# Optimization experiments

Hardware: AMD Instinct MI355X
Metric: run time of the kernel (lower is better)

The kernel has to match this reference:

```python
import jax, jax.numpy as jnp
import numpy as np

# ---- static configuration (mirrors init_kwargs) ----
B, NCAM = 1, 6
FC, FH, FW = 128, 16, 44              # featureShape
ORFH, ORFW = 128, 352                 # transformedImgShape H, W
D_ST, D_END, D_STEP = 1.0, 49.0, 1.0
D = int(np.arange(D_ST, D_END, D_STEP).shape[0])   # 48 depth bins
OUTC = 128
XB = (-50.0, 50.0, 1.0)
YB = (-50.0, 50.0, 1.0)
BEV_H = int((YB[1] - YB[0]) / YB[2])  # 100
BEV_W = int((XB[1] - XB[0]) / XB[2])  # 100
THRESH = 0.05                         # opacity_filter
ERR_TOL = 1.0                         # error_tolerance
COV_DILATE = 0.3                      # 3DGS low-pass on 2D cov diagonal
ALPHA_MAX = 0.99
ALPHA_MIN = 1.0 / 255.0
BN_EPS = 1e-3


def _frustum():
    ds = jnp.arange(D_ST, D_END, D_STEP, dtype=jnp.float32)[:, None, None]
    xs = jnp.linspace(0.0, ORFW - 1.0, FW, dtype=jnp.float32)[None, None, :]
    ys = jnp.linspace(0.0, ORFH - 1.0, FH, dtype=jnp.float32)[None, :, None]
    shp = (D, FH, FW)
    return jnp.stack([jnp.broadcast_to(xs, shp), jnp.broadcast_to(ys, shp),
                      jnp.broadcast_to(ds, shp)], axis=-1)  # [D,FH,FW,3]


def _conv(x, w, b, pad):
    y = jax.lax.conv_general_dilated(x, w, (1, 1), [(pad, pad), (pad, pad)],
                                     dimension_numbers=('NCHW', 'OIHW', 'NCHW'))
    return y + b[None, :, None, None]


def _bn(x, g, beta, m, v):
    # eval-mode BatchNorm2d with running stats
    inv = g / jnp.sqrt(v + BN_EPS)
    return (x - m[None, :, None, None]) * inv[None, :, None, None] + beta[None, :, None, None]


def _rasterize(features, means, cov6, opac):
    """Differentiable BEV Gaussian splatting (alpha compositing in index order).
    features [G,C], means [G,3] (normalized to [-1,1]), cov6 [G,6]=(xx,xy,xz,yy,yz,zz), opac [G].
    """
    h, w = BEV_H, BEV_W
    sh, sw = h / 2.0, w / 2.0                 # h/FoVy, w/FoVx with FoV=2
    op = jnp.where(opac > THRESH, opac, 0.0)  # opacity cull (variable-length mask in torch)
    # full_proj_transform: row0 -> row index (y), row1 -> col index (x)
    py = h / 2.0 - sh * means[:, 1]
    px = w / 2.0 - sw * means[:, 0]
    # 2D covariance in (py,px) basis: J Sigma3 J^T with J = [[0,-sh,0],[-sw,0,0]]
    a = sh * sh * cov6[:, 3] + COV_DILATE     # var along py (from Sigma_yy)
    b = sh * sw * cov6[:, 1]                  # cov(py,px) (from Sigma_xy)
    c = sw * sw * cov6[:, 0] + COV_DILATE     # var along px (from Sigma_xx)
    det = a * c - b * b
    op = jnp.where(det > 0.0, op, 0.0)
    inv_det = 1.0 / jnp.where(det > 0.0, det, 1.0)
    ys = jnp.arange(h, dtype=jnp.float32)
    xs = jnp.arange(w, dtype=jnp.float32)
    dy = py[None, :] - ys[:, None]            # [h,G]
    dx = px[None, :] - xs[:, None]            # [w,G]
    # power = -0.5 d^T Sigma2^{-1} d, Sigma2^{-1} = [[c,-b],[-b,a]]/det
    power = (-0.5 * (c * inv_det) * dy * dy)[:, None, :] \
            + (-0.5 * (a * inv_det) * dx * dx)[None, :, :] \
            + (b * inv_det) * dy[:, None, :] * dx[None, :, :]   # [h,w,G]
    alpha = jnp.minimum(ALPHA_MAX, op * jnp.exp(jnp.minimum(power, 0.0)))
    alpha = jnp.where(alpha < ALPHA_MIN, 0.0, alpha)
    T = jnp.cumprod(1.0 - alpha, axis=-1)
    T_excl = jnp.concatenate([jnp.ones_like(T[..., :1]), T[..., :-1]], axis=-1)
    wgt = alpha * T_excl                      # [h,w,G]
    bev = jnp.einsum('hwg,gc->chw', wgt, features)   # bg color = 0
    return bev


def reference(cam2ego_rot, cam2ego_trans, cam_intrins, post_cam2ego_rot, post_cam2ego_trans,
              img_feats, conv1_w, conv1_b, bn1_g, bn1_b, bn1_m, bn1_v,
              conv2_w, conv2_b, bn2_g, bn2_b, bn2_m, bn2_v, conv3_w, conv3_b):
    # --- geometry lifting ---
    frustum = _frustum()                                             # [D,FH,FW,3]
    pts = frustum[None, None] - post_cam2ego_trans[:, :, None, None, None, :]
    pts = jnp.einsum('bnij,bndhwj->bndhwi', jnp.linalg.inv(post_cam2ego_rot), pts)
    pts = jnp.concatenate([pts[..., :2] * pts[..., 2:3], pts[..., 2:3]], axis=-1)
    combine = cam2ego_rot @ jnp.linalg.inv(cam_intrins)
    geometry = jnp.einsum('bnij,bndhwj->bndhwi', combine, pts) \
               + cam2ego_trans[:, :, None, None, None, :]            # [B,N,D,FH,FW,3]
    # --- depth net ---
    x = img_feats.reshape(B * NCAM, FC, FH, FW)
    x = jax.nn.relu(_bn(_conv(x, conv1_w, conv1_b, 1), bn1_g, bn1_b, bn1_m, bn1_v))
    x = jax.nn.relu(_bn(_conv(x, conv2_w, conv2_b, 1), bn2_g, bn2_b, bn2_m, bn2_v))
    x = _conv(x, conv3_w, conv3_b, 0)                                # [B*N, OUTC+D+1, H, W]
    depth_prob = jax.nn.softmax(x[:, :D], axis=1).reshape(B, NCAM, D, FH, FW)
    opac = jax.nn.sigmoid(x[:, D:D + 1]).reshape(B, NCAM, FH, FW)
    feats = x[:, D + 1:].reshape(B, NCAM, OUTC, FH, FW)
    # --- per-pixel Gaussian moments over the depth distribution ---
    means3d = jnp.einsum('bndhw,bndhwi->bnhwi', depth_prob, geometry)
    delta = means3d[:, :, None] - geometry                           # [B,N,D,FH,FW,3]
    cov = jnp.einsum('bndhw,bndhwi,bndhwj->bnhwij', depth_prob, delta, delta)
    cov = cov * (ERR_TOL ** 2 / 9.0)
    # --- normalize to BEV frame ---
    center = jnp.array([(XB[0] + XB[1]) / 2.0, (YB[0] + YB[1]) / 2.0, 0.0], jnp.float32)
    scale = jnp.array([2.0 / (XB[1] - XB[0]), 2.0 / (YB[1] - YB[0]), 1.0], jnp.float32)
    means_n = (means3d - center) * scale
    cov_n = cov * (scale[:, None] * scale[None, :])
    cov6 = jnp.stack([cov_n[..., 0, 0], cov_n[..., 0, 1], cov_n[..., 0, 2],
                      cov_n[..., 1, 1], cov_n[..., 1, 2], cov_n[..., 2, 2]], axis=-1)
    G = NCAM * FH * FW
    f = jnp.transpose(feats, (0, 1, 3, 4, 2)).reshape(B, G, OUTC)
    m = means_n.reshape(B, G, 3)
    c6 = cov6.reshape(B, G, 6)
    o = opac.reshape(B, G)
    bev = jax.vmap(_rasterize)(f, m, c6, o)                          # [B,OUTC,BEV_H,BEV_W]
    return bev


def setup_inputs() -> dict:
    key = jax.random.key(0)
    ks = jax.random.split(key, 16)
    eye = jnp.eye(3, dtype=jnp.float32)
    cam2ego_rot = eye + 0.05 * jax.random.normal(ks[0], (B, NCAM, 3, 3), jnp.float32)
    cam2ego_trans = 0.5 * jax.random.normal(ks[1], (B, NCAM, 3), jnp.float32)
    intr = jnp.array([[260.0, 0.0, ORFW / 2.0], [0.0, 260.0, ORFH / 2.0], [0.0, 0.0, 1.0]], jnp.float32)
    cam_intrins = jnp.broadcast_to(intr, (B, NCAM, 3, 3)) * (1.0 + 0.01 * jax.random.normal(ks[2], (B, NCAM, 1, 1), jnp.float32))
    post_cam2ego_rot = eye + 0.01 * jax.random.normal(ks[3], (B, NCAM, 3, 3), jnp.float32)
    post_cam2ego_trans = 2.0 * jax.random.normal(ks[4], (B, NCAM, 3), jnp.float32)
    img_feats = jax.random.normal(ks[5], (B, NCAM, FC, FH, FW), jnp.float32)
    def cw(k, o, i, kh, kw):
        return jax.random.normal(k, (o, i, kh, kw), jnp.float32) / np.sqrt(i * kh * kw)
    inp = dict(cam2ego_rot=cam2ego_rot, cam2ego_trans=cam2ego_trans, cam_intrins=cam_intrins,
               post_cam2ego_rot=post_cam2ego_rot, post_cam2ego_trans=post_cam2ego_trans,
               img_feats=img_feats,
               conv1_w=cw(ks[6], FC, FC, 3, 3), conv1_b=jnp.zeros((FC,), jnp.float32),
               bn1_g=jnp.ones((FC,), jnp.float32), bn1_b=0.1 * jax.random.normal(ks[7], (FC,), jnp.float32),
               bn1_m=jnp.zeros((FC,), jnp.float32), bn1_v=jnp.ones((FC,), jnp.float32),
               conv2_w=cw(ks[8], FC, FC, 3, 3), conv2_b=jnp.zeros((FC,), jnp.float32),
               bn2_g=jnp.ones((FC,), jnp.float32), bn2_b=0.1 * jax.random.normal(ks[9], (FC,), jnp.float32),
               bn2_m=jnp.zeros((FC,), jnp.float32), bn2_v=jnp.ones((FC,), jnp.float32),
               conv3_w=cw(ks[10], OUTC + D + 1, FC, 1, 1),
               conv3_b=jnp.zeros((OUTC + D + 1,), jnp.float32))
    return inp
```

## Files before the change

kernel.cpp:

```cpp
#include <hip/hip_runtime.h>
#include <math.h>

#define NCAM 6
#define FHh 16
#define FWw 44
#define PIX 704
#define FCc 128
#define DB 48
#define C3 177
#define KCONV 1152
#define NG 4224
#define BEVN 10000
#define NSPLIT 3
#define SG 1408
#define TH_LOG (-5.5412635f)

#define OFF_WT1    0
#define OFF_WT2    147456
#define OFF_WT3    294912
#define OFF_GEO    319488
#define OFF_X1     724992
#define OFF_X2     1265664
#define OFF_X3     1806336
#define OFF_PART   2553984
#define OFF_PRM    4716672
#define OFF_PRM2   4733568
#define OFF_FEATT  4742016
#define OFF_SF     0
#define OFF_SP     3840000

typedef __attribute__((ext_vector_type(8))) short bf16x8;
typedef __attribute__((ext_vector_type(4))) float f32x4;
typedef __attribute__((ext_vector_type(4))) int i32x4;

__device__ __forceinline__ unsigned short f2bf(float x) {
  unsigned u = __float_as_uint(x);
  return (unsigned short)((u + 0x7FFF + ((u >> 16) & 1)) >> 16);
}
__device__ __forceinline__ float bf2f(unsigned short h) {
  return __uint_as_float(((unsigned)h) << 16);
}

__device__ __forceinline__ void inv3(const float* A, float* I) {
  float a=A[0],b=A[1],c=A[2],d=A[3],e=A[4],f=A[5],g=A[6],h=A[7],i=A[8];
  float c0 = e*i - f*h, c1 = f*g - d*i, c2 = d*h - e*g;
  float det = a*c0 + b*c1 + c*c2;
  float id = 1.f/det;
  I[0]=c0*id; I[1]=(c*h-b*i)*id; I[2]=(b*f-c*e)*id;
  I[3]=c1*id; I[4]=(a*i-c*g)*id; I[5]=(c*d-a*f)*id;
  I[6]=c2*id; I[7]=(b*g-a*h)*id; I[8]=(a*e-b*d)*id;
}

__global__ void k_prep(const float* __restrict__ rot, const float* __restrict__ intr,
                       const float* __restrict__ post_rot,
                       const float* __restrict__ trans, const float* __restrict__ post_trans,
                       const float* __restrict__ w1, const float* __restrict__ w2,
                       const float* __restrict__ w3, float* __restrict__ ws) {
  if (blockIdx.x < 792) {
    __shared__ float sm[NCAM][24];
    if (threadIdx.x < NCAM) {
      int n = threadIdx.x;
      float ip[9], ii[9];
      inv3(post_rot + n*9, ip);
      inv3(intr + n*9, ii);
      const float* R = rot + n*9;
      for (int j = 0; j < 9; ++j) sm[n][j] = ip[j];
      for (int r = 0; r < 3; ++r)
        for (int c = 0; c < 3; ++c) {
          float s = 0.f;
          for (int k = 0; k < 3; ++k) s += R[r*3+k]*ii[k*3+c];
          sm[n][9 + r*3 + c] = s;
        }
    }
    __syncthreads();
    int idx = blockIdx.x*256 + threadIdx.x;
    if (idx >= NCAM*DB*PIX) return;
    int n = idx / (DB*PIX);
    int rem = idx % (DB*PIX);
    int d = rem / PIX;
    int hw = rem % PIX;
    int h = hw / FWw, w = hw % FWw;
    float fx = w * (351.0f/43.0f);
    float fy = h * (127.0f/15.0f);
    float fz = 1.0f + (float)d;
    const float* pt = post_trans + n*3;
    float v0 = fx - pt[0], v1 = fy - pt[1], v2 = fz - pt[2];
    const float* m = sm[n];
    float x = m[0]*v0 + m[1]*v1 + m[2]*v2;
    float y = m[3]*v0 + m[4]*v1 + m[5]*v2;
    float z = m[6]*v0 + m[7]*v1 + m[8]*v2;
    float q0 = x*z, q1 = y*z, q2 = z;
    const float* c = m + 9;
    const float* t = trans + n*3;
    float gx = c[0]*q0 + c[1]*q1 + c[2]*q2 + t[0];
    float gy = c[3]*q0 + c[4]*q1 + c[5]*q2 + t[1];
    ((float2*)(ws + OFF_GEO))[idx] = make_float2(gx, gy);
  } else {
    int e = (blockIdx.x - 792)*256 + threadIdx.x;
    if (e < 147456) {
      float v1 = w1[e], v2 = w2[e];
      unsigned short h1 = f2bf(v1), h2 = f2bf(v2);
      unsigned short l1 = f2bf(v1 - bf2f(h1)), l2 = f2bf(v2 - bf2f(h2));
      unsigned short* wt1 = (unsigned short*)(ws + OFF_WT1);
      unsigned short* wt2 = (unsigned short*)(ws + OFF_WT2);
      wt1[e] = h1; wt1[147456 + e] = l1;
      wt2[e] = h2; wt2[147456 + e] = l2;
    }
    if (e < 192*128) {
      int oc = e >> 7, k = e & 127;
      float v = (oc < C3) ? w3[oc*FCc + k] : 0.f;
      unsigned short h = f2bf(v);
      unsigned short* wt3 = (unsigned short*)(ws + OFF_WT3);
      wt3[e] = h; wt3[24576 + e] = f2bf(v - bf2f(h));
    }
  }
}

#define LROW 20

__global__ __launch_bounds__(256) void k_gemm_mfma(
    const float* __restrict__ in, const float* ws, float* __restrict__ part, int woff)
{
  __shared__ int alds[2][64*LROW];
  __shared__ int blds[2][64*LROW];
  int tid = threadIdx.x;
  int px0 = blockIdx.x * 64;
  int oc0 = blockIdx.y * 64;
  int z = blockIdx.z; int n = z >> 2, ks = z & 3;
  const unsigned short* whi = (const unsigned short*)(ws + woff);
  const unsigned short* wlo = whi + 147456;
  const float* inn = in + (size_t)n*FCc*PIX;
  int wv = tid >> 6, lane = tid & 63;
  int a_oc = tid >> 2, a_kq = tid & 3;
  int b_px = tid & 63, b_kq = tid >> 6;
  int p = px0 + b_px; int b_y = p / FWw, b_x = p - b_y*FWw;
  int k00 = ks * 288;

  i32x4 pa_h, pa_l; float bv[8];
  auto issueA = [&](int s) {
    size_t gi = (size_t)(oc0 + a_oc)*KCONV + (k00 + s*32 + a_kq*8);
    pa_h = *(const i32x4*)(whi + gi);
    pa_l = *(const i32x4*)(wlo + gi);
  };
  auto issueB = [&](int s) {
    #pragma unroll
    for (int j = 0; j < 8; ++j) {
      int k = k00 + s*32 + b_kq*8 + j;
      int ic = k / 9, tap = k - ic*9;
      int ky = tap / 3, kx = tap - ky*3;
      int yy = b_y + ky - 1, xx = b_x + kx - 1;
      float v = 0.f;
      if ((unsigned)yy < FHh && (unsigned)xx < FWw) v = inn[(size_t)ic*PIX + yy*FWw + xx];
      bv[j] = v;
    }
  };

  f32x4 a00 = {0.f,0.f,0.f,0.f}, a01 = a00, a10 = a00, a11 = a00;
  int ocr = (wv >> 1) * 32, pxr = (wv & 1) * 32;
  int dq = (lane >> 4) * 4;
  int rA0 = (ocr + (lane & 15)) * LROW + dq;
  int rA1 = rA0 + 16*LROW;
  int rB0 = (pxr + (lane & 15)) * LROW + dq;
  int rB1 = rB0 + 16*LROW;
  int aw = a_oc*LROW + a_kq*4;
  int bw = b_px*LROW + b_kq*4;

  issueA(0); issueB(0);
  for (int s = 0; s < 9; ++s) {
    __syncthreads();
    *(i32x4*)&alds[0][aw] = pa_h;
    *(i32x4*)&alds[1][aw] = pa_l;
    {
      i32x4 vh, vl;
      int th[8], tl[8];
      #pragma unroll
      for (int j = 0; j < 8; ++j) {
        unsigned short h = f2bf(bv[j]);
        th[j] = h; tl[j] = f2bf(bv[j] - bf2f(h));
      }
      vh.x = th[0]|(th[1]<<16); vh.y = th[2]|(th[3]<<16);
      vh.z = th[4]|(th[5]<<16); vh.w = th[6]|(th[7]<<16);
      vl.x = tl[0]|(tl[1]<<16); vl.y = tl[2]|(tl[3]<<16);
      vl.z = tl[4]|(tl[5]<<16); vl.w = tl[6]|(tl[7]<<16);
      *(i32x4*)&blds[0][bw] = vh;
      *(i32x4*)&blds[1][bw] = vl;
    }
    __syncthreads();
    if (s < 8) { issueA(s+1); issueB(s+1); }
    bf16x8 ah0 = *(bf16x8*)&alds[0][rA0], ah1 = *(bf16x8*)&alds[0][rA1];
    bf16x8 al0 = *(bf16x8*)&alds[1][rA0], al1 = *(bf16x8*)&alds[1][rA1];
    bf16x8 bh0 = *(bf16x8*)&blds[0][rB0], bh1 = *(bf16x8*)&blds[0][rB1];
    bf16x8 bl0 = *(bf16x8*)&blds[1][rB0], bl1 = *(bf16x8*)&blds[1][rB1];
    a00 = __builtin_amdgcn_mfma_f32_16x16x32_bf16(ah0, bh0, a00, 0, 0, 0);
    a01 = __builtin_amdgcn_mfma_f32_16x16x32_bf16(ah0, bh1, a01, 0, 0, 0);
    a10 = __builtin_amdgcn_mfma_f32_16x16x32_bf16(ah1, bh0, a10, 0, 0, 0);
    a11 = __builtin_amdgcn_mfma_f32_16x16x32_bf16(ah1, bh1, a11, 0, 0, 0);
    a00 = __builtin_amdgcn_mfma_f32_16x16x32_bf16(ah0, bl0, a00, 0, 0, 0);
    a01 = __builtin_amdgcn_mfma_f32_16x16x32_bf16(ah0, bl1, a01, 0, 0, 0);
    a10 = __builtin_amdgcn_mfma_f32_16x16x32_bf16(ah1, bl0, a10, 0, 0, 0);
    a11 = __builtin_amdgcn_mfma_f32_16x16x32_bf16(ah1, bl1, a11, 0, 0, 0);
    a00 = __builtin_amdgcn_mfma_f32_16x16x32_bf16(al0, bh0, a00, 0, 0, 0);
    a01 = __builtin_amdgcn_mfma_f32_16x16x32_bf16(al0, bh1, a01, 0, 0, 0);
    a10 = __builtin_amdgcn_mfma_f32_16x16x32_bf16(al1, bh0, a10, 0, 0, 0);
    a11 = __builtin_amdgcn_mfma_f32_16x16x32_bf16(al1, bh1, a11, 0, 0, 0);
  }
  float* pp = part + (size_t)(ks*NCAM + n)*FCc*PIX;
  int ocb = oc0 + ocr + ((lane >> 4) << 2);
  int pxb = px0 + pxr + (lane & 15);
  #pragma unroll
  for (int i = 0; i < 4; ++i) {
    pp[(size_t)(ocb + i)*PIX + pxb]           = a00[i];
    pp[(size_t)(ocb + i)*PIX + pxb + 16]      = a01[i];
    pp[(size_t)(ocb + 16 + i)*PIX + pxb]      = a10[i];
    pp[(size_t)(ocb + 16 + i)*PIX + pxb + 16] = a11[i];
  }
}

__global__ __launch_bounds__(256) void k_gemm_mfma3(
    const float* __restrict__ in, const float* ws,
    const float* __restrict__ bias, float* __restrict__ outbuf)
{
  __shared__ int alds[2][64*LROW];
  __shared__ int blds[2][64*LROW];
  int tid = threadIdx.x;
  int px0 = blockIdx.x * 64;
  int oc0 = blockIdx.y * 64;
  int n = blockIdx.z;
  const unsigned short* whi = (const unsigned short*)(ws + OFF_WT3);
  const unsigned short* wlo = whi + 24576;
  const float* inn = in + (size_t)n*FCc*PIX;
  int wv = tid >> 6, lane = tid & 63;
  int a_oc = tid >> 2, a_kq = tid & 3;
  int b_px = tid & 63, b_kq = tid >> 6;
  int p = px0 + b_px;

  i32x4 pa_h, pa_l; float bvv[8];
  auto issueA = [&](int s) {
    size_t gi = (size_t)(oc0 + a_oc)*128 + (s*32 + a_kq*8);
    pa_h = *(const i32x4*)(whi + gi);
    pa_l = *(const i32x4*)(wlo + gi);
  };
  auto issueB = [&](int s) {
    #pragma unroll
    for (int j = 0; j < 8; ++j) {
      int ic = s*32 + b_kq*8 + j;
      bvv[j] = inn[(size_t)ic*PIX + p];
    }
  };

  f32x4 a00 = {0.f,0.f,0.f,0.f}, a01 = a00, a10 = a00, a11 = a00;
  int ocr = (wv >> 1) * 32, pxr = (wv & 1) * 32;
  int dq = (lane >> 4) * 4;
  int rA0 = (ocr + (lane & 15)) * LROW + dq;
  int rA1 = rA0 + 16*LROW;
  int rB0 = (pxr + (lane & 15)) * LROW + dq;
  int rB1 = rB0 + 16*LROW;
  int aw = a_oc*LROW + a_kq*4;
  int bw = b_px*LROW + b_kq*4;

  issueA(0); issueB(0);
  for (int s = 0; s < 4; ++s) {
    __syncthreads();
    *(i32x4*)&alds[0][aw] = pa_h;
    *(i32x4*)&alds[1][aw] = pa_l;
    {
      i32x4 vh, vl;
      int th[8], tl[8];
      #pragma unroll
      for (int j = 0; j < 8; ++j) {
        unsigned short h = f2bf(bvv[j]);
        th[j] = h; tl[j] = f2bf(bvv[j] - bf2f(h));
      }
      vh.x = th[0]|(th[1]<<16); vh.y = th[2]|(th[3]<<16);
      vh.z = th[4]|(th[5]<<16); vh.w = th[6]|(th[7]<<16);
      vl.x = tl[0]|(tl[1]<<16); vl.y = tl[2]|(tl[3]<<16);
      vl.z = tl[4]|(tl[5]<<16); vl.w = tl[6]|(tl[7]<<16);
      *(i32x4*)&blds[0][bw] = vh;
      *(i32x4*)&blds[1][bw] = vl;
    }
    __syncthreads();
    if (s < 3) { issueA(s+1); issueB(s+1); }
    bf16x8 ah0 = *(bf16x8*)&alds[0][rA0], ah1 = *(bf16x8*)&alds[0][rA1];
    bf16x8 al0 = *(bf16x8*)&alds[1][rA0], al1 = *(bf16x8*)&alds[1][rA1];
    bf16x8 bh0 = *(bf16x8*)&blds[0][rB0], bh1 = *(bf16x8*)&blds[0][rB1];
    bf16x8 bl0 = *(bf16x8*)&blds[1][rB0], bl1 = *(bf16x8*)&blds[1][rB1];
    a00 = __builtin_amdgcn_mfma_f32_16x16x32_bf16(ah0, bh0, a00, 0, 0, 0);
    a01 = __builtin_amdgcn_mfma_f32_16x16x32_bf16(ah0, bh1, a01, 0, 0, 0);
    a10 = __builtin_amdgcn_mfma_f32_16x16x32_bf16(ah1, bh0, a10, 0, 0, 0);
    a11 = __builtin_amdgcn_mfma_f32_16x16x32_bf16(ah1, bh1, a11, 0, 0, 0);
    a00 = __builtin_amdgcn_mfma_f32_16x16x32_bf16(ah0, bl0, a00, 0, 0, 0);
    a01 = __builtin_amdgcn_mfma_f32_16x16x32_bf16(ah0, bl1, a01, 0, 0, 0);
    a10 = __builtin_amdgcn_mfma_f32_16x16x32_bf16(ah1, bl0, a10, 0, 0, 0);
    a11 = __builtin_amdgcn_mfma_f32_16x16x32_bf16(ah1, bl1, a11, 0, 0, 0);
    a00 = __builtin_amdgcn_mfma_f32_16x16x32_bf16(al0, bh0, a00, 0, 0, 0);
    a01 = __builtin_amdgcn_mfma_f32_16x16x32_bf16(al0, bh1, a01, 0, 0, 0);
    a10 = __builtin_amdgcn_mfma_f32_16x16x32_bf16(al1, bh0, a10, 0, 0, 0);
    a11 = __builtin_amdgcn_mfma_f32_16x16x32_bf16(al1, bh1, a11, 0, 0, 0);
  }
  int ocb = oc0 + ocr + ((lane >> 4) << 2);
  int pxb = px0 + pxr + (lane & 15);
  #pragma unroll
  for (int i = 0; i < 4; ++i) {
    int o0 = ocb + i, o1 = ocb + 16 + i;
    if (o0 < C3) {
      float b = bias[o0];
      outbuf[(size_t)(n*C3 + o0)*PIX + pxb]      = a00[i] + b;
      outbuf[(size_t)(n*C3 + o0)*PIX + pxb + 16] = a01[i] + b;
    }
    if (o1 < C3) {
      float b = bias[o1];
      outbuf[(size_t)(n*C3 + o1)*PIX + pxb]      = a10[i] + b;
      outbuf[(size_t)(n*C3 + o1)*PIX + pxb + 16] = a11[i] + b;
    }
  }
}

__global__ void k_epi_bn(const float* __restrict__ part, const float* __restrict__ cb,
                         const float* __restrict__ g, const float* __restrict__ be,
                         const float* __restrict__ mn, const float* __restrict__ vr,
                         float* __restrict__ out, int KSPLIT)
{
  int idx = blockIdx.x*256 + threadIdx.x;
  if (idx >= NCAM*FCc*176) return;
  int px4 = idx % 176;
  int t = idx / 176;
  int oc = t % FCc;
  int n = t / FCc;
  float4 s = {0.f,0.f,0.f,0.f};
  for (int ks = 0; ks < KSPLIT; ++ks) {
    const float4* p = (const float4*)(part + (size_t)((ks*NCAM+n)*FCc + oc)*PIX);
    float4 v = p[px4];
    s.x += v.x; s.y += v.y; s.z += v.z; s.w += v.w;
  }
  float inv = g[oc] * rsqrtf(vr[oc] + 1e-3f);
  float sh = (cb[oc] - mn[oc]) * inv + be[oc];
  float4 o;
  o.x = fmaxf(s.x*inv + sh, 0.f);
  o.y = fmaxf(s.y*inv + sh, 0.f);
  o.z = fmaxf(s.z*inv + sh, 0.f);
  o.w = fmaxf(s.w*inv + sh, 0.f);
  ((float4*)(out + (size_t)(n*FCc + oc)*PIX))[px4] = o;
}

__global__ void k_moments(float* __restrict__ ws) {
  int wid  = (blockIdx.x * 256 + threadIdx.x) >> 6;
  int lane = threadIdx.x & 63;
  int n = wid / PIX, hw = wid % PIX;
  const float* x3 = ws + OFF_X3 + (size_t)n*C3*PIX + hw;
  float logit = (lane < DB) ? x3[(size_t)lane*PIX] : -1e30f;
  float mx = logit;
  for (int off = 1; off < 64; off <<= 1) mx = fmaxf(mx, __shfl_xor(mx, off));
  float e = (lane < DB) ? expf(logit - mx) : 0.f;
  float s = e;
  for (int off = 1; off < 64; off <<= 1) s += __shfl_xor(s, off);
  float p = e / s;
  float gx = 0.f, gy = 0.f;
  if (lane < DB) {
    float2 g2 = ((const float2*)(ws + OFF_GEO))[(size_t)(n*DB + lane)*PIX + hw];
    gx = g2.x; gy = g2.y;
  }
  float sx = p*gx;
  for (int off = 1; off < 64; off <<= 1) sx += __shfl_xor(sx, off);
  float sy = p*gy;
  for (int off = 1; off < 64; off <<= 1) sy += __shfl_xor(sy, off);
  float dx = gx - sx, dy = gy - sy;
  float c00 = p*dx*dx, c01 = p*dx*dy, c11 = p*dy*dy;
  for (int off = 1; off < 64; off <<= 1) c00 += __shfl_xor(c00, off);
  for (int off = 1; off < 64; off <<= 1) c01 += __shfl_xor(c01, off);
  for (int off = 1; off < 64; off <<= 1) c11 += __shfl_xor(c11, off);
  float opl = x3[(size_t)DB*PIX];
  float opac = 1.f / (1.f + expf(-opl));
  float a = c11*(1.f/9.f) + 0.3f;
  float b = c01*(1.f/9.f);
  float c = c00*(1.f/9.f) + 0.3f;
  float py = 50.f - sy;
  float px = 50.f - sx;
  float det = a*c - b*b;
  float op = (opac > 0.05f) ? opac : 0.f;
  float invd = 1.f;
  if (det > 0.f) invd = 1.f/det; else op = 0.f;
  if (lane == 0) {
    float lop = (op > 0.f) ? logf(op) : -1e30f;
    ((float4*)(ws + OFF_PRM))[wid]  = make_float4(py, px, -0.5f*c*invd, -0.5f*a*invd);
    ((float2*)(ws + OFF_PRM2))[wid] = make_float2(b*invd, lop);
  }
  float* ft = ws + OFF_FEATT + (size_t)wid*128;
  ft[lane]      = x3[(size_t)(DB + 1 + lane)*PIX];
  ft[lane + 64] = x3[(size_t)(DB + 1 + lane + 64)*PIX];
}

template<int CTRL, int RMASK>
__device__ __forceinline__ float dpp_mul(float v) {
  int t = __builtin_amdgcn_update_dpp(0x3f800000, __float_as_int(v), CTRL, RMASK, 0xF, false);
  return v * __int_as_float(t);
}

__global__ __launch_bounds__(512) void k_raster(const float* __restrict__ ws,
                                                float* __restrict__ wsout) {
  __shared__ float4 s4[SG];
  __shared__ float2 s2[SG];
  int lane = threadIdx.x & 63, wv = threadIdx.x >> 6;
  int split = blockIdx.x / 1250;
  int pxb   = blockIdx.x % 1250;
  int pix = pxb * 8 + wv;
  float yi = (float)(pix / 100), xi = (float)(pix % 100);
  int gbase = split * SG;
  const float4* prm4 = (const float4*)(ws + OFF_PRM) + gbase;
  const float2* prm2 = (const float2*)(ws + OFF_PRM2) + gbase;
  const float2* ft = (const float2*)(ws + OFF_FEATT);
  for (int i = threadIdx.x; i < SG; i += 512) {
    s4[i] = prm4[i];
    s2[i] = prm2[i];
  }
  __syncthreads();
  float T = 1.f, ax = 0.f, ay = 0.f;
  for (int gl = 0; gl < SG; gl += 64) {
    float4 c4 = s4[gl + lane];
    float2 c2 = s2[gl + lane];
    float dyv = c4.x - yi, dxv = c4.y - xi;
    float pw = c4.z*dyv*dyv + c4.w*dxv*dxv + c2.x*dyv*dxv;
    float t  = pw + c2.y;
    bool hit = (t >= TH_LOG);
    unsigned long long m0 = __ballot(hit);
    if (m0) {
      float alpha = __expf(fminf(t, c2.y));
      alpha = fminf(alpha, 0.99f);
      alpha = hit ? alpha : 0.f;
      float P = 1.f - alpha;
      P = dpp_mul<0x111, 0xF>(P);
      P = dpp_mul<0x112, 0xF>(P);
      P = dpp_mul<0x114, 0xF>(P);
      P = dpp_mul<0x118, 0xF>(P);
      P = dpp_mul<0x142, 0xA>(P);
      P = dpp_mul<0x143, 0xC>(P);
      float E = __int_as_float(__builtin_amdgcn_update_dpp(
                  0x3f800000, __float_as_int(P), 0x138, 0xF, 0xF, false));
      float w = alpha * T * E;
      T *= __int_as_float(__builtin_amdgcn_readlane(__float_as_int(P), 63));
      unsigned long long mask = __ballot(w > 1e-9f);
      int g0 = gbase + gl;
      while (mask) {
        int jj[8];
        #pragma unroll
        for (int b = 0; b < 8; ++b) {
          if (mask) { jj[b] = __builtin_ctzll(mask); mask &= mask - 1ull; }
          else jj[b] = -1;
        }
        float2 fb[8]; float wb[8];
        #pragma unroll
        for (int b = 0; b < 8; ++b) {
          int j = (jj[b] >= 0) ? jj[b] : jj[0];
          fb[b] = ft[(size_t)(g0 + j)*64 + lane];
          wb[b] = (jj[b] >= 0)
            ? __int_as_float(__builtin_amdgcn_readlane(__float_as_int(w), jj[b]))
            : 0.f;
        }
        #pragma unroll
        for (int b = 0; b < 8; ++b) { ax += wb[b]*fb[b].x; ay += wb[b]*fb[b].y; }
      }
      if (T < 1e-7f) break;
    }
  }
  unsigned* sfu = (unsigned*)(wsout + OFF_SF);
  sfu[((size_t)split*BEVN + pix)*64 + lane] =
      (unsigned)f2bf(ax) | ((unsigned)f2bf(ay) << 16);
  if (lane == 0) (wsout + OFF_SP)[split*BEVN + pix] = T;
}

__global__ __launch_bounds__(512) void k_combine(const float* __restrict__ ws,
                                                 float* __restrict__ out) {
  int lane = threadIdx.x & 63, wv = threadIdx.x >> 6;
  int pix = blockIdx.x * 8 + wv;
  const float* sp = ws + OFF_SP;
  float P0 = sp[pix], P1 = sp[BEVN + pix];
  const unsigned* sfu = (const unsigned*)(ws + OFF_SF);
  unsigned u0 = sfu[(size_t)pix*64 + lane];
  unsigned u1 = sfu[((size_t)BEVN + pix)*64 + lane];
  unsigned u2 = sfu[((size_t)2*BEVN + pix)*64 + lane];
  float w1 = P0, w2 = P0*P1;
  float ox = bf2f((unsigned short)(u0 & 0xffff))
           + w1*bf2f((unsigned short)(u1 & 0xffff))
           + w2*bf2f((unsigned short)(u2 & 0xffff));
  float oy = bf2f((unsigned short)(u0 >> 16))
           + w1*bf2f((unsigned short)(u1 >> 16))
           + w2*bf2f((unsigned short)(u2 >> 16));
  out[(size_t)(2*lane)*BEVN + pix]   = ox;
  out[(size_t)(2*lane+1)*BEVN + pix] = oy;
}

extern "C" void kernel_launch(void* const* d_in, const int* in_sizes, int n_in,
                              void* d_out, int out_size, void* d_ws, size_t ws_size,
                              hipStream_t stream) {
  const float* rot        = (const float*)d_in[0];
  const float* trans      = (const float*)d_in[1];
  const float* intr       = (const float*)d_in[2];
  const float* post_rot   = (const float*)d_in[3];
  const float* post_trans = (const float*)d_in[4];
  const float* img        = (const float*)d_in[5];
  const float* w1  = (const float*)d_in[6];
  const float* b1  = (const float*)d_in[7];
  const float* g1  = (const float*)d_in[8];
  const float* be1 = (const float*)d_in[9];
  const float* m1  = (const float*)d_in[10];
  const float* v1  = (const float*)d_in[11];
  const float* w2  = (const float*)d_in[12];
  const float* b2  = (const float*)d_in[13];
  const float* g2  = (const float*)d_in[14];
  const float* be2 = (const float*)d_in[15];
  const float* m2  = (const float*)d_in[16];
  const float* v2  = (const float*)d_in[17];
  const float* w3  = (const float*)d_in[18];
  const float* b3  = (const float*)d_in[19];
  float* ws  = (float*)d_ws;
  float* out = (float*)d_out;

  k_prep<<<1368, 256, 0, stream>>>(rot, intr, post_rot, trans, post_trans,
                                   w1, w2, w3, ws);

  k_gemm_mfma<<<dim3(11,2,24), 256, 0, stream>>>(img, ws, ws+OFF_PART, OFF_WT1);
  k_epi_bn<<<528, 256, 0, stream>>>(ws+OFF_PART, b1, g1, be1, m1, v1, ws+OFF_X1, 4);
  k_gemm_mfma<<<dim3(11,2,24), 256, 0, stream>>>(ws+OFF_X1, ws, ws+OFF_PART, OFF_WT2);
  k_epi_bn<<<528, 256, 0, stream>>>(ws+OFF_PART, b2, g2, be2, m2, v2, ws+OFF_X2, 4);
  k_gemm_mfma3<<<dim3(11,3,6), 256, 0, stream>>>(ws+OFF_X2, ws, b3, ws+OFF_X3);

  k_moments<<<1056, 256, 0, stream>>>(ws);
  k_raster<<<3750, 512, 0, stream>>>(ws, ws);
  k_combine<<<1250, 512, 0, stream>>>(ws, out);
}
```

Measured before the change: 119.8 us.

## Restructure moments kernel to pixel-per-lane with coalesced loads and LDS transpose

The moments kernel now maps 64 consecutive pixels to lanes and splits the 48 depth bins across 4 waves. Softmax and moment reductions go through shared memory instead of 64-lane shuffle trees, and the feature transpose is staged through an LDS tile so both the reads and the writes are coalesced. This removes the strided per-wave gathers and the many shuffle reductions. The trade-off is that the grid drops from 1056 blocks to 66, so fewer CUs are occupied.

```diff
diff --git a/kernel.cpp b/kernel.cpp
--- a/kernel.cpp
+++ b/kernel.cpp
@@ -342,51 +342,85 @@
   ((float4*)(out + (size_t)(n*FCc + oc)*PIX))[px4] = o;
 }
 
-__global__ void k_moments(float* __restrict__ ws) {
-  int wid  = (blockIdx.x * 256 + threadIdx.x) >> 6;
-  int lane = threadIdx.x & 63;
-  int n = wid / PIX, hw = wid % PIX;
-  const float* x3 = ws + OFF_X3 + (size_t)n*C3*PIX + hw;
-  float logit = (lane < DB) ? x3[(size_t)lane*PIX] : -1e30f;
-  float mx = logit;
-  for (int off = 1; off < 64; off <<= 1) mx = fmaxf(mx, __shfl_xor(mx, off));
-  float e = (lane < DB) ? expf(logit - mx) : 0.f;
-  float s = e;
-  for (int off = 1; off < 64; off <<= 1) s += __shfl_xor(s, off);
-  float p = e / s;
-  float gx = 0.f, gy = 0.f;
-  if (lane < DB) {
-    float2 g2 = ((const float2*)(ws + OFF_GEO))[(size_t)(n*DB + lane)*PIX + hw];
-    gx = g2.x; gy = g2.y;
-  }
-  float sx = p*gx;
-  for (int off = 1; off < 64; off <<= 1) sx += __shfl_xor(sx, off);
-  float sy = p*gy;
-  for (int off = 1; off < 64; off <<= 1) sy += __shfl_xor(sy, off);
-  float dx = gx - sx, dy = gy - sy;
-  float c00 = p*dx*dx, c01 = p*dx*dy, c11 = p*dy*dy;
-  for (int off = 1; off < 64; off <<= 1) c00 += __shfl_xor(c00, off);
-  for (int off = 1; off < 64; off <<= 1) c01 += __shfl_xor(c01, off);
-  for (int off = 1; off < 64; off <<= 1) c11 += __shfl_xor(c11, off);
-  float opl = x3[(size_t)DB*PIX];
-  float opac = 1.f / (1.f + expf(-opl));
-  float a = c11*(1.f/9.f) + 0.3f;
-  float b = c01*(1.f/9.f);
-  float c = c00*(1.f/9.f) + 0.3f;
-  float py = 50.f - sy;
-  float px = 50.f - sx;
-  float det = a*c - b*b;
-  float op = (opac > 0.05f) ? opac : 0.f;
-  float invd = 1.f;
-  if (det > 0.f) invd = 1.f/det; else op = 0.f;
-  if (lane == 0) {
+__global__ __launch_bounds__(256) void k_moments(float* __restrict__ ws) {
+  __shared__ float r0[4][64], r1[4][64], r2[4][64];
+  __shared__ float tile[64][65];
+  int tid = threadIdx.x;
+  int w = tid >> 6, l = tid & 63;
+  int n = blockIdx.x / 11, hw0 = (blockIdx.x % 11) * 64;
+  int hw = hw0 + l;
+  const float* x3 = ws + OFF_X3 + (size_t)n*C3*PIX;
+  const float2* geo = (const float2*)(ws + OFF_GEO);
+  float le[12], gxr[12], gyr[12];
+  float pm = -1e30f;
+  #pragma unroll
+  for (int j = 0; j < 12; ++j) {
+    le[j] = x3[(size_t)(w*12 + j)*PIX + hw];
+    pm = fmaxf(pm, le[j]);
+  }
+  r0[w][l] = pm;
+  __syncthreads();
+  float mx = fmaxf(fmaxf(r0[0][l], r0[1][l]), fmaxf(r0[2][l], r0[3][l]));
+  __syncthreads();
+  float s_p = 0.f, sx_p = 0.f, sy_p = 0.f;
+  #pragma unroll
+  for (int j = 0; j < 12; ++j) {
+    float e = expf(le[j] - mx);
+    le[j] = e;
+    float2 g2 = geo[(size_t)(n*DB + w*12 + j)*PIX + hw];
+    gxr[j] = g2.x; gyr[j] = g2.y;
+    s_p += e; sx_p += e*g2.x; sy_p += e*g2.y;
+  }
+  r0[w][l] = s_p; r1[w][l] = sx_p; r2[w][l] = sy_p;
+  __syncthreads();
+  float s  = r0[0][l] + r0[1][l] + r0[2][l] + r0[3][l];
+  float sx = (r1[0][l] + r1[1][l] + r1[2][l] + r1[3][l]) / s;
+  float sy = (r2[0][l] + r2[1][l] + r2[2][l] + r2[3][l]) / s;
+  __syncthreads();
+  float cxx = 0.f, cxy = 0.f, cyy = 0.f;
+  #pragma unroll
+  for (int j = 0; j < 12; ++j) {
+    float dx = gxr[j] - sx, dy = gyr[j] - sy;
+    cxx += le[j]*dx*dx; cxy += le[j]*dx*dy; cyy += le[j]*dy*dy;
+  }
+  r0[w][l] = cxx; r1[w][l] = cxy; r2[w][l] = cyy;
+  __syncthreads();
+  if (w == 0) {
+    float c00 = (r0[0][l] + r0[1][l] + r0[2][l] + r0[3][l]) / s;
+    float c01 = (r1[0][l] + r1[1][l] + r1[2][l] + r1[3][l]) / s;
+    float c11 = (r2[0][l] + r2[1][l] + r2[2][l] + r2[3][l]) / s;
+    float opl = x3[(size_t)DB*PIX + hw];
+    float opac = 1.f / (1.f + expf(-opl));
+    float a = c11*(1.f/9.f) + 0.3f;
+    float b = c01*(1.f/9.f);
+    float c = c00*(1.f/9.f) + 0.3f;
+    float py = 50.f - sy;
+    float px = 50.f - sx;
+    float det = a*c - b*b;
+    float op = (opac > 0.05f) ? opac : 0.f;
+    float invd = 1.f;
+    if (det > 0.f) invd = 1.f/det; else op = 0.f;
     float lop = (op > 0.f) ? logf(op) : -1e30f;
+    int wid = n*PIX + hw;
     ((float4*)(ws + OFF_PRM))[wid]  = make_float4(py, px, -0.5f*c*invd, -0.5f*a*invd);
     ((float2*)(ws + OFF_PRM2))[wid] = make_float2(b*invd, lop);
   }
-  float* ft = ws + OFF_FEATT + (size_t)wid*128;
-  ft[lane]      = x3[(size_t)(DB + 1 + lane)*PIX];
-  ft[lane + 64] = x3[(size_t)(DB + 1 + lane + 64)*PIX];
+  float* ft = ws + OFF_FEATT;
+  for (int half = 0; half < 2; ++half) {
+    __syncthreads();
+    int ch0 = half*64;
+    #pragma unroll
+    for (int r = 0; r < 16; ++r) {
+      int ch = w*16 + r;
+      tile[ch][l] = x3[(size_t)(DB + 1 + ch0 + ch)*PIX + hw];
+    }
+    __syncthreads();
+    #pragma unroll
+    for (int k = 0; k < 16; ++k) {
+      int h = w + 4*k;
+      ft[(size_t)(n*PIX + hw0 + h)*128 + ch0 + l] = tile[l][h];
+    }
+  }
 }
 
 template<int CTRL, int RMASK>
@@ -523,7 +557,7 @@
   k_epi_bn<<<528, 256, 0, stream>>>(ws+OFF_PART, b2, g2, be2, m2, v2, ws+OFF_X2, 4);
   k_gemm_mfma3<<<dim3(11,3,6), 256, 0, stream>>>(ws+OFF_X2, ws, b3, ws+OFF_X3);
 
-  k_moments<<<1056, 256, 0, stream>>>(ws);
+  k_moments<<<66, 256, 0, stream>>>(ws);
   k_raster<<<3750, 512, 0, stream>>>(ws, ws);
   k_combine<<<1250, 512, 0, stream>>>(ws, out);
 }
```

After: 118.4 us. Within noise of the previous version (-1.2%).
